# Performance work log

Measured on AMD Instinct MI355X. Metric: run time of the kernel, lower is better.

## Reference

```python
import jax, jax.numpy as jnp
import numpy as np
from jax import lax

HIDDEN = 64


def setup_inputs() -> dict:
    key = jax.random.key(0)
    ks = jax.random.split(key, 8)
    B, T, C, H, W = 8, 16, 3, 64, 64
    x = jax.random.normal(ks[0], (B, T, C, H, W), dtype=jnp.float32)
    # SE-style attention 1x1 convs (no bias): fc1 3->1, fc2 1->3
    att_w1 = jax.random.normal(ks[1], (1, 3), dtype=jnp.float32) * 0.5
    att_w2 = jax.random.normal(ks[2], (3, 1), dtype=jnp.float32) * 0.5
    # ConvLSTM layer 0: in = 3 + 64 = 67, out = 4*64 gates, 3x3 kernel
    conv_w0 = jax.random.normal(ks[3], (4 * HIDDEN, 3 + HIDDEN, 3, 3), dtype=jnp.float32) * 0.05
    conv_b0 = jnp.zeros((4 * HIDDEN,), dtype=jnp.float32)
    # ConvLSTM layer 1: in = 64 + 64 = 128
    conv_w1 = jax.random.normal(ks[4], (4 * HIDDEN, 2 * HIDDEN, 3, 3), dtype=jnp.float32) * 0.05
    conv_b1 = jnp.zeros((4 * HIDDEN,), dtype=jnp.float32)
    return {"x": x, "att_w1": att_w1, "att_w2": att_w2,
            "conv_w0": conv_w0, "conv_b0": conv_b0,
            "conv_w1": conv_w1, "conv_b1": conv_b1}


def _attention_scale(x, w1, w2):
    # x: [B, T, C, H, W] -> channel attention per timestep, vectorized over B,T
    avg = x.mean(axis=(-2, -1))          # [B, T, C]
    mx = x.max(axis=(-2, -1))            # [B, T, C]
    def fc(v):
        return jnp.einsum('or,btr->bto', w2, jax.nn.relu(jnp.einsum('rc,btc->btr', w1, v)))
    return jax.nn.sigmoid(fc(avg) + fc(mx))  # [B, T, C]


def _convlstm_layer(xseq, w, b, hidden):
    # xseq: [B, T, Cin, H, W]; returns ([B, T, hidden, H, W], h_last, c_last)
    B, T, Cin, H, W = xseq.shape
    h0 = jnp.zeros((B, hidden, H, W), xseq.dtype)
    c0 = jnp.zeros((B, hidden, H, W), xseq.dtype)

    def step(carry, xt):
        h, c = carry
        comb = jnp.concatenate([xt, h], axis=1)  # [B, Cin+hidden, H, W]
        conv = lax.conv_general_dilated(
            comb, w, window_strides=(1, 1), padding='SAME',
            dimension_numbers=('NCHW', 'OIHW', 'NCHW')) + b[None, :, None, None]
        cc_i, cc_f, cc_o, cc_g = jnp.split(conv, 4, axis=1)
        c_new = jax.nn.sigmoid(cc_f) * c + jax.nn.sigmoid(cc_i) * jnp.tanh(cc_g)
        h_new = jax.nn.sigmoid(cc_o) * jnp.tanh(c_new)
        return (h_new, c_new), h_new

    (h_last, c_last), hs = lax.scan(step, (h0, c0), jnp.moveaxis(xseq, 1, 0))
    return jnp.moveaxis(hs, 0, 1), h_last, c_last


def reference(x, att_w1, att_w2, conv_w0, conv_b0, conv_w1, conv_b1):
    # attention gating (broadcast [B,T,C,1,1] over H,W as in torch broadcast assign)
    scale = _attention_scale(x, att_w1, att_w2)
    xin = x * scale[..., None, None]
    out0, _, _ = _convlstm_layer(xin, conv_w0, conv_b0, HIDDEN)
    out1, h1, c1 = _convlstm_layer(out0, conv_w1, conv_b1, HIDDEN)
    # return_all_layers=False: last layer output + its final state
    return out1, h1, c1
```

## Files before the change

kernel.cpp:

```cpp
#include <hip/hip_runtime.h>
#include <hip/hip_bf16.h>
#include <math.h>

#define HW 4096
#define NB 8
#define NT 16

typedef unsigned short u16;
typedef __attribute__((ext_vector_type(8))) short bf16x8;
typedef __attribute__((ext_vector_type(4))) float f32x4;

__device__ __forceinline__ float sigmoid_f(float x) {
  return 1.f / (1.f + __expf(-x));
}
__device__ __forceinline__ float tanh_f(float x) {
  float ax = fabsf(x);
  float e = __expf(2.f * ax);
  float t = 1.f - 2.f / (e + 1.f);
  return copysignf(t, x);
}
__device__ __forceinline__ u16 f2b(float v) {
  __hip_bfloat16 h = __float2bfloat16(v);
  return *(u16*)&h;
}

__global__ void transform_wB(const float* __restrict__ w, u16* __restrict__ wtB,
                             int CIN, int cinbase, int nch) {
  int idx = blockIdx.x * 256 + threadIdx.x;
  int total = nch * 9 * 256 * 32;
  if (idx >= total) return;
  int ci32 = idx & 31;
  int rest = idx >> 5;
  int gate = rest & 255;
  rest >>= 8;
  int tap = rest % 9;
  int chunk = rest / 9;
  int cin = cinbase + chunk * 32 + ci32;
  wtB[idx] = f2b(w[((size_t)gate * CIN + cin) * 9 + tap]);
}

__global__ void transform_wA(const float* __restrict__ w0, u16* __restrict__ wtA) {
  int idx = blockIdx.x * 256 + threadIdx.x;
  if (idx >= 8192) return;
  int k = idx & 31, gate = idx >> 5;
  u16 v = 0;
  if (k < 27) {
    int ci = (k >= 18) + (k >= 9);
    int tap = k - ci * 9;
    v = f2b(w0[((size_t)gate * 67 + ci) * 9 + tap]);
  }
  wtA[idx] = v;
}

__global__ void att_reduce(const float* __restrict__ x, float* __restrict__ avg,
                           float* __restrict__ mx) {
  int btc = blockIdx.x;
  const float* p = x + (size_t)btc * HW;
  float s = 0.f, m = -INFINITY;
  for (int i = threadIdx.x; i < HW; i += 256) {
    float v = p[i];
    s += v;
    m = fmaxf(m, v);
  }
  #pragma unroll
  for (int off = 32; off; off >>= 1) {
    s += __shfl_down(s, off, 64);
    m = fmaxf(m, __shfl_down(m, off, 64));
  }
  __shared__ float ss[4], sm[4];
  int wid = threadIdx.x >> 6, lane = threadIdx.x & 63;
  if (lane == 0) { ss[wid] = s; sm[wid] = m; }
  __syncthreads();
  if (threadIdx.x == 0) {
    avg[btc] = (ss[0] + ss[1] + ss[2] + ss[3]) * (1.f / 4096.f);
    mx[btc]  = fmaxf(fmaxf(sm[0], sm[1]), fmaxf(sm[2], sm[3]));
  }
}

__global__ void att_apply(const float* __restrict__ x, const float* __restrict__ avg,
                          const float* __restrict__ mx, const float* __restrict__ w1,
                          const float* __restrict__ w2, u16* __restrict__ xin_t) {
  size_t i = (size_t)blockIdx.x * 256 + threadIdx.x;
  int pix = (int)(i & 4095);
  int c   = (int)((i >> 12) % 3);
  int bt  = (int)(i / (3 * HW));
  const float* a = avg + bt * 3;
  const float* m = mx + bt * 3;
  float ra = fmaxf(0.f, w1[0] * a[0] + w1[1] * a[1] + w1[2] * a[2]);
  float rm = fmaxf(0.f, w1[0] * m[0] + w1[1] * m[1] + w1[2] * m[2]);
  float sc = sigmoid_f(w2[c] * (ra + rm));
  xin_t[((size_t)bt * HW + pix) * 4 + c] = f2b(x[i] * sc);
}

struct RoleP {
  const u16* a0; long a0_bs; const u16* wtA;
  const u16* s0; long s0_bs; int s0_ch;
  const u16* s1; long s1_bs; int s1_ch;
  const u16* wtB; const float* bias;
  float* c_t;
  u16* h_t;
  float* out_f32; long out_bs;
};

__device__ __forceinline__ void dma_site(const u16* sp, u16* bufn, int idx,
                                         const u16* zb, int r0) {
  int site = idx >> 2, sub = idx & 3;
  int r = site / 66, cc = site - r * 66;
  int gr = r0 - 1 + r, gc = cc - 1;
  const u16* g = ((unsigned)gr < 64u && (unsigned)gc < 64u)
               ? sp + (size_t)(gr * 64 + gc) * 32 + sub * 8
               : zb;
  u16* l = bufn + (size_t)(idx & ~63) * 8;
  __builtin_amdgcn_global_load_lds(
      (const __attribute__((address_space(1))) unsigned int*)g,
      (__attribute__((address_space(3))) unsigned int*)l, 16, 0, 0);
}

__device__ __forceinline__ void dma_chunk(const u16* sp, u16* bufn, const u16* zb,
                                          int r0, int tid) {
  #pragma unroll
  for (int it = 0; it < 3; ++it) dma_site(sp, bufn, it * 256 + tid, zb, r0);
  if (tid < 64) dma_site(sp, bufn, 768 + tid, zb, r0);
}

#define BQ_LOAD(S, BASE, TP)                                              \
  { _Pragma("unroll")                                                     \
    for (int _g = 0; _g < 4; ++_g)                                        \
      bq[S][_g] = *(const bf16x8*)((BASE) + (TP) * 8192 + _g * 2048); }

template <int PAR>
__device__ __forceinline__ void chunk_compute(const u16* bufc, const u16* bpc,
                                              const u16* bpn, bool more,
                                              bf16x8 (&bq)[2][4], f32x4 (&acc)[4][4],
                                              int abase) {
  #pragma unroll
  for (int tap = 0; tap < 9; ++tap) {
    if (tap < 8) { BQ_LOAD((tap + 1 + PAR) & 1, bpc, tap + 1) }
    else if (more) { BQ_LOAD((1 + PAR) & 1, bpn, 0) }
    const int dy = tap / 3, dx = tap - dy * 3;
    bf16x8 av[4];
    #pragma unroll
    for (int mt = 0; mt < 4; ++mt)
      av[mt] = *(const bf16x8*)(bufc + (dy * 66 + dx + mt * 16) * 32 + abase);
    #pragma unroll
    for (int mt = 0; mt < 4; ++mt)
      #pragma unroll
      for (int gt = 0; gt < 4; ++gt)
        acc[mt][gt] = __builtin_amdgcn_mfma_f32_16x16x32_bf16(
            av[mt], bq[(tap + PAR) & 1][gt], acc[mt][gt], 0, 0, 0);
  }
}

#define SP_SET(CG)                                                           \
  sp = ((CG) < P.s0_ch)                                                      \
     ? P.s0 + (size_t)b * P.s0_bs + (size_t)(CG) * 131072                    \
     : P.s1 + (size_t)b * P.s1_bs + (size_t)((CG) - P.s0_ch) * 131072;

__global__ __launch_bounds__(256, 4) void conv_step(
    RoleP r0p, RoleP r1p, int zbase, const u16* __restrict__ zb)
{
  __shared__ __align__(16) u16 smem[2][6656];
  __shared__ __align__(16) u16 xtile[2048];
  const RoleP P = (blockIdx.z + zbase) ? r1p : r0p;
  const int r0 = blockIdx.x, b = blockIdx.y;
  const int tid = threadIdx.x;
  const int w = tid >> 6, lane = tid & 63;
  const int n = lane & 15, q = lane >> 4;
  const int abase = n * 32 + q * 8;
  const int ntot = P.s0_ch + P.s1_ch;

  f32x4 acc[4][4];
  #pragma unroll
  for (int mt = 0; mt < 4; ++mt)
    #pragma unroll
    for (int gt = 0; gt < 4; ++gt)
      acc[mt][gt] = (f32x4){0.f, 0.f, 0.f, 0.f};

  const u16* bp0 = P.wtB + (size_t)(w * 16 + n) * 32 + q * 8;
  bf16x8 bq[2][4];
  const u16* sp;

  SP_SET(0);
  dma_chunk(sp, &smem[0][0], zb, r0, tid);
  BQ_LOAD(0, bp0, 0)
  if (P.a0) {
    const u16* ap = P.a0 + (size_t)b * P.a0_bs;
    for (int idx = tid; idx < 2048; idx += 256) {
      int k = idx & 31, px = idx >> 5;
      u16 v = 0;
      if (k < 27) {
        int ci = (k >= 18) + (k >= 9);
        int tap = k - ci * 9;
        int dy = (tap >= 6) ? 2 : (tap >= 3 ? 1 : 0);
        int dx = tap - dy * 3;
        int gr = r0 - 1 + dy, gc = px - 1 + dx;
        if ((unsigned)gr < 64u && (unsigned)gc < 64u)
          v = ap[((size_t)(gr * 64 + gc)) * 4 + ci];
      }
      xtile[idx] = v;
    }
  }
  __syncthreads();
  if (P.a0) {
    bf16x8 bxa[4], axv[4];
    #pragma unroll
    for (int gt = 0; gt < 4; ++gt)
      bxa[gt] = *(const bf16x8*)(P.wtA + ((w + 4 * gt) * 16 + n) * 32 + q * 8);
    #pragma unroll
    for (int mt = 0; mt < 4; ++mt)
      axv[mt] = *(const bf16x8*)(xtile + (mt * 16 + n) * 32 + q * 8);
    #pragma unroll
    for (int mt = 0; mt < 4; ++mt)
      #pragma unroll
      for (int gt = 0; gt < 4; ++gt)
        acc[mt][gt] = __builtin_amdgcn_mfma_f32_16x16x32_bf16(axv[mt], bxa[gt], acc[mt][gt], 0, 0, 0);
  }

  int cur = 0;
  for (int cg = 0; cg < ntot; cg += 2) {
    {
      SP_SET(cg + 1);
      dma_chunk(sp, &smem[cur ^ 1][0], zb, r0, tid);
      chunk_compute<0>(&smem[cur][0], bp0 + (size_t)cg * 73728,
                       bp0 + (size_t)(cg + 1) * 73728, true, bq, acc, abase);
      __syncthreads();
      cur ^= 1;
    }
    {
      bool more = (cg + 2 < ntot);
      if (more) {
        SP_SET(cg + 2);
        dma_chunk(sp, &smem[cur ^ 1][0], zb, r0, tid);
      }
      chunk_compute<1>(&smem[cur][0], bp0 + (size_t)(cg + 1) * 73728,
                       bp0 + (size_t)(cg + 2) * 73728, more, bq, acc, abase);
      __syncthreads();
      cur ^= 1;
    }
  }

  const int hc = w * 16 + n;
  const float bi = P.bias[hc], bfv = P.bias[64 + hc], bo = P.bias[128 + hc], bg = P.bias[192 + hc];
  float* cB = P.c_t + ((size_t)b * HW + r0 * 64) * 64 + hc;
  u16*   hB = P.h_t + (size_t)b * 262144 + (size_t)(hc >> 5) * 131072
            + (size_t)(r0 * 64) * 32 + (hc & 31);
  float* tbuf = (float*)&smem[0][0];
  #pragma unroll
  for (int mt = 0; mt < 4; ++mt) {
    #pragma unroll
    for (int reg = 0; reg < 4; ++reg) {
      int px = mt * 16 + q * 4 + reg;
      float xi = acc[mt][0][reg] + bi;
      float xf = acc[mt][1][reg] + bfv;
      float xo = acc[mt][2][reg] + bo;
      float xg = acc[mt][3][reg] + bg;
      float ii = sigmoid_f(xi), ff = sigmoid_f(xf), oo = sigmoid_f(xo), gg = tanh_f(xg);
      float cold = cB[(size_t)px * 64];
      float cnew = ff * cold + ii * gg;
      float hnew = oo * tanh_f(cnew);
      cB[(size_t)px * 64] = cnew;
      hB[(size_t)px * 32] = f2b(hnew);
      if (P.out_f32) tbuf[px * 65 + hc] = hnew;
    }
  }
  if (P.out_f32) {
    __syncthreads();
    int hc2 = tid >> 2, qq = tid & 3;
    float* orow = P.out_f32 + (size_t)b * P.out_bs + (size_t)hc2 * HW + r0 * 64;
    #pragma unroll
    for (int j = 0; j < 4; ++j) {
      int p0x = qq * 4 + j * 16;
      float4 v = make_float4(tbuf[(p0x + 0) * 65 + hc2], tbuf[(p0x + 1) * 65 + hc2],
                             tbuf[(p0x + 2) * 65 + hc2], tbuf[(p0x + 3) * 65 + hc2]);
      *(float4*)(orow + p0x) = v;
    }
  }
}

__global__ void h1_final(const float* __restrict__ out1, float* __restrict__ dst) {
  size_t i = (size_t)blockIdx.x * 256 + threadIdx.x;
  size_t b = i >> 18, rem = i & 262143;
  dst[i] = out1[(b * NT + (NT - 1)) * 262144 + rem];
}

__global__ void c1_final(const float* __restrict__ c_t, float* __restrict__ dst) {
  __shared__ float t[64][65];
  int pb = blockIdx.x, b = blockIdx.y;
  int tx = threadIdx.x & 63, ty = threadIdx.x >> 6;
  for (int i = 0; i < 16; ++i) {
    int p = i * 4 + ty;
    t[p][tx] = c_t[((size_t)b * HW + pb * 64 + p) * 64 + tx];
  }
  __syncthreads();
  for (int i = 0; i < 16; ++i) {
    int hcv = i * 4 + ty;
    dst[(size_t)b * 262144 + (size_t)hcv * HW + pb * 64 + tx] = t[tx][hcv];
  }
}

extern "C" void kernel_launch(void* const* d_in, const int* in_sizes, int n_in,
                              void* d_out, int out_size, void* d_ws, size_t ws_size,
                              hipStream_t stream) {
  const float* x      = (const float*)d_in[0];
  const float* att_w1 = (const float*)d_in[1];
  const float* att_w2 = (const float*)d_in[2];
  const float* w0     = (const float*)d_in[3];
  const float* b0     = (const float*)d_in[4];
  const float* w1     = (const float*)d_in[5];
  const float* b1     = (const float*)d_in[6];
  float* out = (float*)d_out;
  char* ws = (char*)d_ws;

  u16*   xin_t = (u16*)(ws + 0);
  u16*   h0a   = (u16*)(ws + 4194304);
  u16*   h0b   = (u16*)(ws + 8388608);
  u16*   h1a   = (u16*)(ws + 12582912);
  u16*   h1b   = (u16*)(ws + 16777216);
  u16*   zb    = (u16*)(ws + 20971520);
  u16*   wtA0  = (u16*)(ws + 21495808);
  u16*   wtB0  = (u16*)(ws + 21512192);
  u16*   wtB1  = (u16*)(ws + 21807104);
  float* c0_t  = (float*)(ws + 22396928);
  float* c1_t  = (float*)(ws + 30785536);
  float* avg   = (float*)(ws + 39174144);
  float* mxb   = (float*)(ws + 39175680);
  if (ws_size < 39177216u) return;

  hipMemsetAsync(xin_t, 0, 4194304, stream);
  hipMemsetAsync(zb, 0, 524288, stream);
  hipMemsetAsync(c0_t, 0, 8388608, stream);
  hipMemsetAsync(c1_t, 0, 8388608, stream);

  transform_wA<<<32, 256, 0, stream>>>(w0, wtA0);
  transform_wB<<<576, 256, 0, stream>>>(w0, wtB0, 67, 3, 2);
  transform_wB<<<1152, 256, 0, stream>>>(w1, wtB1, 128, 0, 4);
  att_reduce<<<NB * NT * 3, 256, 0, stream>>>(x, avg, mxb);
  att_apply<<<1572864 / 256, 256, 0, stream>>>(x, avg, mxb, att_w1, att_w2, xin_t);

  const long HB = 262144;

  for (int s = 0; s <= NT; ++s) {
    bool has0 = (s < NT), has1 = (s > 0);
    RoleP p0 = {}, p1 = {};
    if (has0) {
      int t = s;
      p0.a0 = xin_t + (size_t)t * 16384; p0.a0_bs = (long)NT * 16384; p0.wtA = wtA0;
      p0.s0 = (t == 0) ? zb : ((t & 1) ? h0a : h0b);
      p0.s0_bs = (t == 0) ? 0L : HB; p0.s0_ch = 2;
      p0.s1 = zb; p0.s1_bs = 0L; p0.s1_ch = 0;
      p0.wtB = wtB0; p0.bias = b0; p0.c_t = c0_t;
      p0.h_t = (t & 1) ? h0b : h0a;
      p0.out_f32 = (float*)0; p0.out_bs = 0L;
    }
    if (has1) {
      int t = s - 1;
      p1.a0 = (const u16*)0; p1.a0_bs = 0L; p1.wtA = (const u16*)0;
      p1.s0 = (t & 1) ? h0b : h0a;
      p1.s0_bs = HB; p1.s0_ch = 2;
      p1.s1 = (t == 0) ? zb : ((t & 1) ? h1a : h1b);
      p1.s1_bs = (t == 0) ? 0L : HB; p1.s1_ch = 2;
      p1.wtB = wtB1; p1.bias = b1; p1.c_t = c1_t;
      p1.h_t = (t & 1) ? h1b : h1a;
      p1.out_f32 = out + (size_t)t * 262144; p1.out_bs = (long)NT * 262144;
    }
    int zbase = has0 ? 0 : 1;
    int zn = (has0 && has1) ? 2 : 1;
    conv_step<<<dim3(64, 8, zn), 256, 0, stream>>>(p0, p1, zbase, zb);
  }

  h1_final<<<8192, 256, 0, stream>>>(out, out + 33554432);
  c1_final<<<dim3(64, 8), 256, 0, stream>>>(c1_t, out + 35651584);
}
```

Baseline: 933.7 us.

## Compute two output rows per block to share haloed input tile

Result: no change. 918.8 us (-1.6%).

```diff
diff --git a/kernel.cpp b/kernel.cpp
--- a/kernel.cpp
+++ b/kernel.cpp
@@ -103,11 +103,11 @@
 };
 
 __device__ __forceinline__ void dma_site(const u16* sp, u16* bufn, int idx,
-                                         const u16* zb, int r0) {
+                                         const u16* zb, int r0g) {
   int site = idx >> 2, sub = idx & 3;
   int r = site / 66, cc = site - r * 66;
-  int gr = r0 - 1 + r, gc = cc - 1;
-  const u16* g = ((unsigned)gr < 64u && (unsigned)gc < 64u)
+  int gr = r0g - 1 + r, gc = cc - 1;
+  const u16* g = (site < 264 && (unsigned)gr < 64u && (unsigned)gc < 64u)
                ? sp + (size_t)(gr * 64 + gc) * 32 + sub * 8
                : zb;
   u16* l = bufn + (size_t)(idx & ~63) * 8;
@@ -117,10 +117,10 @@
 }
 
 __device__ __forceinline__ void dma_chunk(const u16* sp, u16* bufn, const u16* zb,
-                                          int r0, int tid) {
-  #pragma unroll
-  for (int it = 0; it < 3; ++it) dma_site(sp, bufn, it * 256 + tid, zb, r0);
-  if (tid < 64) dma_site(sp, bufn, 768 + tid, zb, r0);
+                                          int r0g, int tid) {
+  #pragma unroll
+  for (int it = 0; it < 2; ++it) dma_site(sp, bufn, it * 512 + tid, zb, r0g);
+  if (tid < 64) dma_site(sp, bufn, 1024 + tid, zb, r0g);
 }
 
 #define BQ_LOAD(S, BASE, TP)                                              \
@@ -132,7 +132,7 @@
 __device__ __forceinline__ void chunk_compute(const u16* bufc, const u16* bpc,
                                               const u16* bpn, bool more,
                                               bf16x8 (&bq)[2][4], f32x4 (&acc)[4][4],
-                                              int abase) {
+                                              int abase2) {
   #pragma unroll
   for (int tap = 0; tap < 9; ++tap) {
     if (tap < 8) { BQ_LOAD((tap + 1 + PAR) & 1, bpc, tap + 1) }
@@ -141,7 +141,7 @@
     bf16x8 av[4];
     #pragma unroll
     for (int mt = 0; mt < 4; ++mt)
-      av[mt] = *(const bf16x8*)(bufc + (dy * 66 + dx + mt * 16) * 32 + abase);
+      av[mt] = *(const bf16x8*)(bufc + abase2 + dy * 2112 + dx * 32 + mt * 512);
     #pragma unroll
     for (int mt = 0; mt < 4; ++mt)
       #pragma unroll
@@ -156,17 +156,18 @@
      ? P.s0 + (size_t)b * P.s0_bs + (size_t)(CG) * 131072                    \
      : P.s1 + (size_t)b * P.s1_bs + (size_t)((CG) - P.s0_ch) * 131072;
 
-__global__ __launch_bounds__(256, 4) void conv_step(
+__global__ __launch_bounds__(512, 4) void conv_step(
     RoleP r0p, RoleP r1p, int zbase, const u16* __restrict__ zb)
 {
-  __shared__ __align__(16) u16 smem[2][6656];
-  __shared__ __align__(16) u16 xtile[2048];
+  __shared__ __align__(16) u16 smem[2][8704];
+  __shared__ __align__(16) u16 xtile[4096];
   const RoleP P = (blockIdx.z + zbase) ? r1p : r0p;
-  const int r0 = blockIdx.x, b = blockIdx.y;
+  const int r0g = blockIdx.x * 2, b = blockIdx.y;
   const int tid = threadIdx.x;
   const int w = tid >> 6, lane = tid & 63;
   const int n = lane & 15, q = lane >> 4;
-  const int abase = n * 32 + q * 8;
+  const int gc = w >> 1, mh = w & 1;
+  const int abase2 = mh * 2112 + n * 32 + q * 8;
   const int ntot = P.s0_ch + P.s1_ch;
 
   f32x4 acc[4][4];
@@ -176,26 +177,27 @@
     for (int gt = 0; gt < 4; ++gt)
       acc[mt][gt] = (f32x4){0.f, 0.f, 0.f, 0.f};
 
-  const u16* bp0 = P.wtB + (size_t)(w * 16 + n) * 32 + q * 8;
+  const u16* bp0 = P.wtB + (size_t)(gc * 16 + n) * 32 + q * 8;
   bf16x8 bq[2][4];
   const u16* sp;
 
   SP_SET(0);
-  dma_chunk(sp, &smem[0][0], zb, r0, tid);
+  dma_chunk(sp, &smem[0][0], zb, r0g, tid);
   BQ_LOAD(0, bp0, 0)
   if (P.a0) {
     const u16* ap = P.a0 + (size_t)b * P.a0_bs;
-    for (int idx = tid; idx < 2048; idx += 256) {
-      int k = idx & 31, px = idx >> 5;
+    for (int idx = tid; idx < 4096; idx += 512) {
+      int row = idx >> 11, rest = idx & 2047;
+      int k = rest & 31, px = rest >> 5;
       u16 v = 0;
       if (k < 27) {
         int ci = (k >= 18) + (k >= 9);
         int tap = k - ci * 9;
         int dy = (tap >= 6) ? 2 : (tap >= 3 ? 1 : 0);
         int dx = tap - dy * 3;
-        int gr = r0 - 1 + dy, gc = px - 1 + dx;
-        if ((unsigned)gr < 64u && (unsigned)gc < 64u)
-          v = ap[((size_t)(gr * 64 + gc)) * 4 + ci];
+        int gr = r0g + row - 1 + dy, gcl = px - 1 + dx;
+        if ((unsigned)gr < 64u && (unsigned)gcl < 64u)
+          v = ap[((size_t)(gr * 64 + gcl)) * 4 + ci];
       }
       xtile[idx] = v;
     }
@@ -205,10 +207,10 @@
     bf16x8 bxa[4], axv[4];
     #pragma unroll
     for (int gt = 0; gt < 4; ++gt)
-      bxa[gt] = *(const bf16x8*)(P.wtA + ((w + 4 * gt) * 16 + n) * 32 + q * 8);
+      bxa[gt] = *(const bf16x8*)(P.wtA + ((gc + 4 * gt) * 16 + n) * 32 + q * 8);
     #pragma unroll
     for (int mt = 0; mt < 4; ++mt)
-      axv[mt] = *(const bf16x8*)(xtile + (mt * 16 + n) * 32 + q * 8);
+      axv[mt] = *(const bf16x8*)(xtile + mh * 2048 + (mt * 16 + n) * 32 + q * 8);
     #pragma unroll
     for (int mt = 0; mt < 4; ++mt)
       #pragma unroll
@@ -220,9 +222,9 @@
   for (int cg = 0; cg < ntot; cg += 2) {
     {
       SP_SET(cg + 1);
-      dma_chunk(sp, &smem[cur ^ 1][0], zb, r0, tid);
+      dma_chunk(sp, &smem[cur ^ 1][0], zb, r0g, tid);
       chunk_compute<0>(&smem[cur][0], bp0 + (size_t)cg * 73728,
-                       bp0 + (size_t)(cg + 1) * 73728, true, bq, acc, abase);
+                       bp0 + (size_t)(cg + 1) * 73728, true, bq, acc, abase2);
       __syncthreads();
       cur ^= 1;
     }
@@ -230,20 +232,21 @@
       bool more = (cg + 2 < ntot);
       if (more) {
         SP_SET(cg + 2);
-        dma_chunk(sp, &smem[cur ^ 1][0], zb, r0, tid);
+        dma_chunk(sp, &smem[cur ^ 1][0], zb, r0g, tid);
       }
       chunk_compute<1>(&smem[cur][0], bp0 + (size_t)(cg + 1) * 73728,
-                       bp0 + (size_t)(cg + 2) * 73728, more, bq, acc, abase);
+                       bp0 + (size_t)(cg + 2) * 73728, more, bq, acc, abase2);
       __syncthreads();
       cur ^= 1;
     }
   }
 
-  const int hc = w * 16 + n;
+  const int hc = gc * 16 + n;
+  const int orow_g = r0g + mh;
   const float bi = P.bias[hc], bfv = P.bias[64 + hc], bo = P.bias[128 + hc], bg = P.bias[192 + hc];
-  float* cB = P.c_t + ((size_t)b * HW + r0 * 64) * 64 + hc;
+  float* cB = P.c_t + ((size_t)b * HW + orow_g * 64) * 64 + hc;
   u16*   hB = P.h_t + (size_t)b * 262144 + (size_t)(hc >> 5) * 131072
-            + (size_t)(r0 * 64) * 32 + (hc & 31);
+            + (size_t)(orow_g * 64) * 32 + (hc & 31);
   float* tbuf = (float*)&smem[0][0];
   #pragma unroll
   for (int mt = 0; mt < 4; ++mt) {
@@ -260,18 +263,20 @@
       float hnew = oo * tanh_f(cnew);
       cB[(size_t)px * 64] = cnew;
       hB[(size_t)px * 32] = f2b(hnew);
-      if (P.out_f32) tbuf[px * 65 + hc] = hnew;
+      if (P.out_f32) tbuf[(mh * 64 + px) * 65 + hc] = hnew;
     }
   }
   if (P.out_f32) {
     __syncthreads();
-    int hc2 = tid >> 2, qq = tid & 3;
-    float* orow = P.out_f32 + (size_t)b * P.out_bs + (size_t)hc2 * HW + r0 * 64;
+    int hc2 = (tid >> 2) & 63, qq = tid & 3, rw = tid >> 8;
+    float* orow = P.out_f32 + (size_t)b * P.out_bs + (size_t)hc2 * HW + (r0g + rw) * 64;
     #pragma unroll
     for (int j = 0; j < 4; ++j) {
       int p0x = qq * 4 + j * 16;
-      float4 v = make_float4(tbuf[(p0x + 0) * 65 + hc2], tbuf[(p0x + 1) * 65 + hc2],
-                             tbuf[(p0x + 2) * 65 + hc2], tbuf[(p0x + 3) * 65 + hc2]);
+      float4 v = make_float4(tbuf[(rw * 64 + p0x + 0) * 65 + hc2],
+                             tbuf[(rw * 64 + p0x + 1) * 65 + hc2],
+                             tbuf[(rw * 64 + p0x + 2) * 65 + hc2],
+                             tbuf[(rw * 64 + p0x + 3) * 65 + hc2]);
       *(float4*)(orow + p0x) = v;
     }
   }
@@ -365,7 +370,7 @@
     }
     int zbase = has0 ? 0 : 1;
     int zn = (has0 && has1) ? 2 : 1;
-    conv_step<<<dim3(64, 8, zn), 256, 0, stream>>>(p0, p1, zbase, zb);
+    conv_step<<<dim3(32, 8, zn), 512, 0, stream>>>(p0, p1, zbase, zb);
   }
 
   h1_final<<<8192, 256, 0, stream>>>(out, out + 33554432);
```
